# Kernel optimization log

Measured on AMD Instinct MI355X. Metric: run time of the kernel, lower is better.

Reference implementation:

```python
import jax, jax.numpy as jnp
import numpy as np

# Hyperparameters from init_kwargs (linear beta schedule, is_lin=True branch)
BETA_1 = 1e-4
BETA_T = 0.02
T = 1000
B = 8192
IMG = 32


def _schedule_coeffs():
    """Closed-form coefficients for the original's per-sample iterative loop.

    The original recursion (iterative_process) is, for iter = 0..t-1:
        x_{k+1} = x_k * s_k + normal * (beta_k^2 * I)
    where s_k = sqrt_alphas_bar[k] (NB: the original multiplies by the
    *cumulative* sqrt-alpha at every step, and the 'std' is beta^2 * eye(32)
    broadcast over channels). Unrolling gives
        x_t = x_0 * P_t + normal * I * C_t
    with P_t = prod_{k<t} s_k and C_t = sum_{k<t} beta_k^2 * prod_{k<j<t} s_j,
    which satisfy P_{t} = P_{t-1}*s_{t-1}, C_t = C_{t-1}*s_{t-1} + beta_{t-1}^2.
    """
    betas = jnp.linspace(BETA_1, BETA_T, T + 1, dtype=jnp.float32)
    alphas_cumprod = jnp.cumprod(1.0 - betas)
    s = jnp.sqrt(alphas_cumprod)          # sqrt_alphas_bar, shape (T+1,)
    P = jnp.cumprod(s)                    # P[k] = P_{t=k+1}

    def step(c, xs):
        s_k, b_k = xs
        c = c * s_k + b_k * b_k
        return c, c

    _, C = jax.lax.scan(step, jnp.float32(0.0), (s, betas))  # C[k] = C_{t=k+1}
    return P, C


def setup_inputs() -> dict:
    key = jax.random.key(0)
    k1, k2, k3 = jax.random.split(key, 3)
    x_0 = jax.random.uniform(k1, (B, 3, IMG, IMG), dtype=jnp.float32)
    normal = jax.random.normal(k2, (B, 3, IMG, IMG), dtype=jnp.float32)
    # original: torch.randint(low=1, high=T+1, size=(B,))
    timesteps = jax.random.randint(k3, (B,), 1, T + 1, dtype=jnp.int32)
    return {"x_0": x_0, "normal": normal, "timesteps": timesteps}


def reference(x_0, normal, timesteps):
    P, C = _schedule_coeffs()
    idx = timesteps - 1                   # t in [1, T] -> array index t-1
    Pt = P[idx][:, None, None, None]      # (B,1,1,1)
    Ct = C[idx][:, None, None, None]      # (B,1,1,1)
    eye = jnp.eye(IMG, dtype=x_0.dtype)   # diagonal mask from beta*eye(32)
    # x_t = x_0 * P_t + normal * (C_t * I), broadcast over (B,3,32,32)
    x_t = x_0 * Pt + normal * eye * Ct
    return x_t
```

## Files before the change

### kernel.cpp

```cpp
#include <hip/hip_runtime.h>


constexpr int T_STEPS = 1000;
constexpr int BATCH   = 8192;
constexpr int N_ELEM  = BATCH * 3 * 32 * 32;
constexpr int NF4     = N_ELEM / 4;

struct Tables { float P[T_STEPS]; float C[T_STEPS]; };

constexpr double csqrt_d(double x) {
    if (x <= 0.0) return 0.0;
    double scale = 1.0;
    while (x < 0.25) { x *= 4.0;  scale *= 0.5; }
    while (x >= 1.0) { x *= 0.25; scale *= 2.0; }
    double g = 0.5 * (x + 1.0);
    for (int i = 0; i < 40; ++i) {
        double ng = 0.5 * (g + x / g);
        if (ng == g) break;
        g = ng;
    }
    return g * scale;
}

constexpr Tables make_tables() {
    Tables t{};
    const float beta1 = 1e-4f;
    const float betaT = 0.02f;
    const float delta = (betaT - beta1) / 1000.0f;
    float ac = 1.0f, P = 1.0f, c = 0.0f;
    for (int k = 0; k < T_STEPS; ++k) {
        float beta = beta1 + (float)k * delta;
        ac = ac * (1.0f - beta);
        float s = (float)csqrt_d((double)ac);
        P = P * s;
        c = c * s + beta * beta;
        t.P[k] = P;
        t.C[k] = c;
    }
    return t;
}

__device__ __constant__ Tables d_tbl = make_tables();

__global__ __launch_bounds__(256) void gaussian_diffusion_kernel(
    const float* __restrict__ x0,
    const float* __restrict__ nrm,
    const int*   __restrict__ tsteps,
    float*       __restrict__ out)
{
    int f = blockIdx.x * 256 + threadIdx.x;
    if (f >= NF4) return;
    int e   = f << 2;
    int b   = e / 3072;
    int rem = e - b * 3072;
    int p   = rem & 1023;
    int h   = p >> 5;
    int w0  = p & 31;

    int   t  = tsteps[b] - 1;
    float Pt = d_tbl.P[t];
    float Ct = d_tbl.C[t];

    const float4 x = reinterpret_cast<const float4*>(x0)[f];

    int   d  = h - w0;
    float nv = 0.0f;
    if ((unsigned)d < 4u) nv = nrm[e + d] * Ct;

    float4 r;
    r.x = x.x * Pt + (d == 0 ? nv : 0.0f);
    r.y = x.y * Pt + (d == 1 ? nv : 0.0f);
    r.z = x.z * Pt + (d == 2 ? nv : 0.0f);
    r.w = x.w * Pt + (d == 3 ? nv : 0.0f);

    reinterpret_cast<float4*>(out)[f] = r;
}

extern "C" void kernel_launch(void* const* d_in, const int* in_sizes, int n_in,
                              void* d_out, int out_size, void* d_ws, size_t ws_size,
                              hipStream_t stream) {
    const float* x0     = (const float*)d_in[0];
    const float* nrm    = (const float*)d_in[1];
    const int*   tsteps = (const int*)d_in[2];
    float*       out    = (float*)d_out;

    const int blocks = NF4 / 256;
    gaussian_diffusion_kernel<<<blocks, 256, 0, stream>>>(x0, nrm, tsteps, out);
}
```

Baseline: 239.9 us.

## Process four images per block with shared per-image coefficients

Each block now handles four whole images (12 float4 per thread) instead of one float4 per thread. The per-image P/C coefficients are loaded once into shared memory, and the per-element divide and index math is replaced by fixed per-thread diagonal offsets. This cuts block count, index arithmetic and per-thread timestep and table lookups. In exchange it adds a __syncthreads and gives fewer, larger blocks, which may reduce the memory parallelism available to this bandwidth-bound kernel.

Result: slower. 250.1 us (+4.2%).

```diff
diff --git a/kernel.cpp b/kernel.cpp
--- a/kernel.cpp
+++ b/kernel.cpp
@@ -3,8 +3,9 @@
 
 constexpr int T_STEPS = 1000;
 constexpr int BATCH   = 8192;
-constexpr int N_ELEM  = BATCH * 3 * 32 * 32;
-constexpr int NF4     = N_ELEM / 4;
+constexpr int IMGS_PER_BLOCK = 4;
+constexpr int F4_PER_IMG     = 768;
+constexpr int BLOCKS = BATCH / IMGS_PER_BLOCK;
 
 struct Tables { float P[T_STEPS]; float C[T_STEPS]; };
 
@@ -42,38 +43,56 @@
 
 __device__ __constant__ Tables d_tbl = make_tables();
 
-__global__ __launch_bounds__(256) void gaussian_diffusion_kernel(
+__global__ __launch_bounds__(256, 4) void gaussian_diffusion_kernel(
     const float* __restrict__ x0,
     const float* __restrict__ nrm,
     const int*   __restrict__ tsteps,
     float*       __restrict__ out)
 {
-    int f = blockIdx.x * 256 + threadIdx.x;
-    if (f >= NF4) return;
-    int e   = f << 2;
-    int b   = e / 3072;
-    int rem = e - b * 3072;
-    int p   = rem & 1023;
-    int h   = p >> 5;
-    int w0  = p & 31;
+    __shared__ float2 s_coef[IMGS_PER_BLOCK];
 
-    int   t  = tsteps[b] - 1;
-    float Pt = d_tbl.P[t];
-    float Ct = d_tbl.C[t];
+    const int tid = threadIdx.x;
+    const int b0  = blockIdx.x * IMGS_PER_BLOCK;
 
-    const float4 x = reinterpret_cast<const float4*>(x0)[f];
+    if (tid < IMGS_PER_BLOCK) {
+        int t = tsteps[b0 + tid] - 1;
+        s_coef[tid] = make_float2(d_tbl.P[t], d_tbl.C[t]);
+    }
+    __syncthreads();
 
-    int   d  = h - w0;
-    float nv = 0.0f;
-    if ((unsigned)d < 4u) nv = nrm[e + d] * Ct;
+    const float2 c0 = s_coef[0];
+    const float2 c1 = s_coef[1];
+    const float2 c2 = s_coef[2];
+    const float2 c3 = s_coef[3];
 
-    float4 r;
-    r.x = x.x * Pt + (d == 0 ? nv : 0.0f);
-    r.y = x.y * Pt + (d == 1 ? nv : 0.0f);
-    r.z = x.z * Pt + (d == 2 ? nv : 0.0f);
-    r.w = x.w * Pt + (d == 3 ? nv : 0.0f);
+    const int h  = tid >> 3;
+    const int w0 = (tid & 7) << 2;
+    const int d  = h - w0;
+    const bool has_diag = (unsigned)d < 4u;
 
-    reinterpret_cast<float4*>(out)[f] = r;
+    const int base = b0 * F4_PER_IMG;
+    const float4* __restrict__ x4 = reinterpret_cast<const float4*>(x0);
+    float4*       __restrict__ o4 = reinterpret_cast<float4*>(out);
+
+    #pragma unroll
+    for (int j = 0; j < 12; ++j) {
+        const int img = j / 3;
+        const float Pt = (img == 0) ? c0.x : (img == 1) ? c1.x : (img == 2) ? c2.x : c3.x;
+        const float Ct = (img == 0) ? c0.y : (img == 1) ? c1.y : (img == 2) ? c2.y : c3.y;
+
+        const int gf4 = base + j * 256 + tid;
+        const float4 x = x4[gf4];
+
+        float nv = 0.0f;
+        if (has_diag) nv = nrm[(gf4 << 2) + d] * Ct;
+
+        float4 r;
+        r.x = x.x * Pt + (d == 0 ? nv : 0.0f);
+        r.y = x.y * Pt + (d == 1 ? nv : 0.0f);
+        r.z = x.z * Pt + (d == 2 ? nv : 0.0f);
+        r.w = x.w * Pt + (d == 3 ? nv : 0.0f);
+        o4[gf4] = r;
+    }
 }
 
 extern "C" void kernel_launch(void* const* d_in, const int* in_sizes, int n_in,
@@ -84,6 +103,5 @@
     const int*   tsteps = (const int*)d_in[2];
     float*       out    = (float*)d_out;
 
-    const int blocks = NF4 / 256;
-    gaussian_diffusion_kernel<<<blocks, 256, 0, stream>>>(x0, nrm, tsteps, out);
+    gaussian_diffusion_kernel<<<BLOCKS, 256, 0, stream>>>(x0, nrm, tsteps, out);
 }
```

## Split into dense scale kernel and sparse diagonal noise-add kernel

Applied to the files above, without the earlier changes.

Replaces the single fused kernel with two launches. The first streams x0 and writes x0*P_t for every element with no per-element index math. The second touches only the 32 diagonal elements per channel image and adds normal*C_t in place. This simplifies the index arithmetic and branching in the bulk pass. In exchange it adds a second launch plus scattered read-modify-write traffic on the diagonal, which the original already handled inside the fused pass.

New measurement: 256.0 us. +6.7%, slower.

```diff
diff --git a/kernel.cpp b/kernel.cpp
--- a/kernel.cpp
+++ b/kernel.cpp
@@ -3,8 +3,9 @@
 
 constexpr int T_STEPS = 1000;
 constexpr int BATCH   = 8192;
-constexpr int N_ELEM  = BATCH * 3 * 32 * 32;
-constexpr int NF4     = N_ELEM / 4;
+constexpr int K1_BLOCKS  = BATCH * 3;
+constexpr int N_DIAG     = BATCH * 3 * 32;
+constexpr int K2_BLOCKS  = N_DIAG / 256;
 
 struct Tables { float P[T_STEPS]; float C[T_STEPS]; };
 
@@ -42,38 +43,40 @@
 
 __device__ __constant__ Tables d_tbl = make_tables();
 
-__global__ __launch_bounds__(256) void gaussian_diffusion_kernel(
+__global__ __launch_bounds__(256) void scale_kernel(
     const float* __restrict__ x0,
+    const int*   __restrict__ tsteps,
+    float*       __restrict__ out)
+{
+    const int bid = blockIdx.x;
+    const int img = bid / 3;
+    const int t   = tsteps[img] - 1;
+    const float Pt = d_tbl.P[t];
+
+    const int f = bid * 256 + threadIdx.x;
+    const float4 x = reinterpret_cast<const float4*>(x0)[f];
+    float4 r;
+    r.x = x.x * Pt;
+    r.y = x.y * Pt;
+    r.z = x.z * Pt;
+    r.w = x.w * Pt;
+    reinterpret_cast<float4*>(out)[f] = r;
+}
+
+__global__ __launch_bounds__(256) void diag_kernel(
     const float* __restrict__ nrm,
     const int*   __restrict__ tsteps,
     float*       __restrict__ out)
 {
-    int f = blockIdx.x * 256 + threadIdx.x;
-    if (f >= NF4) return;
-    int e   = f << 2;
-    int b   = e / 3072;
-    int rem = e - b * 3072;
-    int p   = rem & 1023;
-    int h   = p >> 5;
-    int w0  = p & 31;
+    const int gid = blockIdx.x * 256 + threadIdx.x;
+    const int img = gid / 96;
+    const int rem = gid - img * 96;
+    const int off = img * 3072 + rem * 32 + (rem & 31);
 
-    int   t  = tsteps[b] - 1;
-    float Pt = d_tbl.P[t];
-    float Ct = d_tbl.C[t];
+    const int t    = tsteps[img] - 1;
+    const float Ct = d_tbl.C[t];
 
-    const float4 x = reinterpret_cast<const float4*>(x0)[f];
-
-    int   d  = h - w0;
-    float nv = 0.0f;
-    if ((unsigned)d < 4u) nv = nrm[e + d] * Ct;
-
-    float4 r;
-    r.x = x.x * Pt + (d == 0 ? nv : 0.0f);
-    r.y = x.y * Pt + (d == 1 ? nv : 0.0f);
-    r.z = x.z * Pt + (d == 2 ? nv : 0.0f);
-    r.w = x.w * Pt + (d == 3 ? nv : 0.0f);
-
-    reinterpret_cast<float4*>(out)[f] = r;
+    out[off] = fmaf(nrm[off], Ct, out[off]);
 }
 
 extern "C" void kernel_launch(void* const* d_in, const int* in_sizes, int n_in,
@@ -84,6 +87,6 @@
     const int*   tsteps = (const int*)d_in[2];
     float*       out    = (float*)d_out;
 
-    const int blocks = NF4 / 256;
-    gaussian_diffusion_kernel<<<blocks, 256, 0, stream>>>(x0, nrm, tsteps, out);
+    scale_kernel<<<K1_BLOCKS, 256, 0, stream>>>(x0, tsteps, out);
+    diag_kernel <<<K2_BLOCKS, 256, 0, stream>>>(nrm, tsteps, out);
 }
```
